# Kernel optimization log

Hardware: AMD Instinct MI355X
Metric: run time of the kernel (lower is better)

## Reference

```python
import jax, jax.numpy as jnp
import numpy as np

NUM_HEADS = 12
ROPE_THETA = 10000.0


def rope_angles(hd, end_x, end_y):
    # axial 2D rope angles, shape (L, hd//2); first hd//4 from x-coord, next hd//4 from y-coord
    f = 1.0 / (ROPE_THETA ** (np.arange(0, hd, 4)[: hd // 4].astype(np.float32) / hd))
    t = np.arange(end_x * end_y)
    tx = (t % end_x).astype(np.float32)
    ty = (t // end_x).astype(np.float32)
    ang = np.concatenate([np.outer(tx, f), np.outer(ty, f)], axis=-1)
    return jnp.asarray(ang, dtype=jnp.float32)


def apply_rope(q, ang):
    # q: (B, nH, L, hd); complex multiply on adjacent pairs
    cos, sin = jnp.cos(ang), jnp.sin(ang)  # (L, hd//2)
    qr = q.reshape(*q.shape[:-1], -1, 2)
    a, b = qr[..., 0], qr[..., 1]
    return jnp.stack([a * cos - b * sin, a * sin + b * cos], axis=-1).reshape(q.shape)


def setup_inputs() -> dict:
    key = jax.random.key(0)
    ks = jax.random.split(key, 7)
    dim, H, W, B = 768, 32, 32, 8
    hd = dim // NUM_HEADS
    return {
        "x": jax.random.normal(ks[0], (B, H, W, dim), jnp.float32),
        "qkv_w": jax.random.normal(ks[1], (3 * dim, dim), jnp.float32) * 0.02,
        "qkv_b": jax.random.normal(ks[2], (3 * dim,), jnp.float32) * 0.02,
        "proj_w": jax.random.normal(ks[3], (dim, dim), jnp.float32) * 0.02,
        "proj_b": jax.random.normal(ks[4], (dim,), jnp.float32) * 0.02,
        "rel_pos_h": jax.random.normal(ks[5], (2 * H - 1, hd), jnp.float32) * 0.02,
        "rel_pos_w": jax.random.normal(ks[6], (2 * W - 1, hd), jnp.float32) * 0.02,
    }


def reference(x, qkv_w, qkv_b, proj_w, proj_b, rel_pos_h, rel_pos_w):
    B, H, W, dim = x.shape
    nH = NUM_HEADS
    hd = dim // nH
    L = H * W
    qkv = jnp.einsum("blc,dc->bld", x.reshape(B, L, dim), qkv_w) + qkv_b
    qkv = qkv.reshape(B, L, 3, nH, hd)
    q = qkv[:, :, 0].transpose(0, 2, 1, 3)  # (B, nH, L, hd)
    k = qkv[:, :, 1].transpose(0, 2, 1, 3)
    v = qkv[:, :, 2].transpose(0, 2, 1, 3)
    # 2D rope (applied to both q and k)
    ang = rope_angles(hd, H, W)
    q = apply_rope(q, ang)
    k = apply_rope(k, ang)
    # relative position bias: equivalent math of concat_rel_pos(rescale=True) + SDPA
    # effective scores = (q.k)/sqrt(hd) + rel_h + rel_w
    rc = jnp.arange(H)[:, None] - jnp.arange(W)[None, :] + (H - 1)  # (H, W)
    Rh = rel_pos_h[rc]  # (H, K_h, hd)
    Rw = rel_pos_w[rc]  # (W, K_w, hd)
    rq = q.reshape(B, nH, H, W, hd)
    rel_h = jnp.einsum("bnhwc,hkc->bnhwk", rq, Rh)  # (B, nH, H, W, K_h)
    rel_w = jnp.einsum("bnhwc,wkc->bnhwk", rq, Rw)  # (B, nH, H, W, K_w)
    scores = jnp.einsum("bnqc,bnkc->bnqk", q, k) / jnp.sqrt(jnp.float32(hd))
    scores = scores.reshape(B, nH, H, W, H, W) + rel_h[..., :, None] + rel_w[..., None, :]
    attn = jax.nn.softmax(scores.reshape(B, nH, L, L), axis=-1)
    out = jnp.einsum("bnqk,bnkc->bnqc", attn, v)  # (B, nH, L, hd)
    out = out.transpose(0, 2, 1, 3).reshape(B, H, W, dim)
    return jnp.einsum("bhwc,dc->bhwd", out, proj_w) + proj_b
```

## Files before the change

kernel.cpp:

```cpp
#include <hip/hip_runtime.h>


typedef unsigned short u16;
typedef __attribute__((ext_vector_type(8))) __bf16 bf16x8;
typedef __attribute__((ext_vector_type(4))) float f32x4;
typedef __attribute__((address_space(1))) const unsigned int gu32;
typedef __attribute__((address_space(3))) unsigned int lu32;

#define LOG2E 1.4426950408889634f

__device__ __forceinline__ float b2f(u16 u) {
    unsigned int i = ((unsigned int)u) << 16;
    float f; __builtin_memcpy(&f, &i, 4); return f;
}
__device__ __forceinline__ u16 f2b(float f) {
    unsigned int x; __builtin_memcpy(&x, &f, 4);
    x += 0x7fffu + ((x >> 16) & 1u);
    return (u16)(x >> 16);
}

#define LDT 72

__global__ void detect_dtype(const u16* __restrict__ x, int* __restrict__ flag)
{
    if (threadIdx.x == 0 && blockIdx.x == 0) {
        float mx = 0.f;
        for (int i = 0; i < 128; i++) {
            float v = fabsf(b2f(x[i]));
            if (!(v <= 1e30f)) v = 1e30f;
            mx = fmaxf(mx, v);
        }
        *flag = (mx > 1e4f) ? 1 : 0;
    }
}

struct CvtArgs {
    const void* src[7];
    u16*        dst[7];
    int         n[7];
    float       sc[7];
};

__global__ __launch_bounds__(256) void convert_all(CvtArgs a, const int* __restrict__ flag)
{
    const int fl = *flag;
    const int g = blockIdx.x * 256 + threadIdx.x;
    const int stride = gridDim.x * 256;
    #pragma unroll 1
    for (int s = 0; s < 7; s++) {
        const int n = a.n[s];
        const float sc = a.sc[s];
        const float* fs = (const float*)a.src[s];
        const u16*  hs = (const u16*)a.src[s];
        u16* d = a.dst[s];
        for (int i = g; i < n; i += stride) {
            float v = fl ? fs[i] : b2f(hs[i]);
            d[i] = f2b(v * sc);
        }
    }
}

template <int EPI>
__global__ __launch_bounds__(256) void gemm128(
    const u16* __restrict__ A, const u16* __restrict__ Bw,
    const u16* __restrict__ bias, void* __restrict__ Cout,
    const int* __restrict__ flag, u16* __restrict__ qkvT, int N, int K)
{
    __shared__ __align__(16) u16 smem[16384];
    u16* lA = smem;
    u16* lB = smem + 8192;
    u16* ct = smem;
    const int tid = threadIdx.x;
    const int m0 = blockIdx.x * 128, n0 = blockIdx.y * 128;
    const int wave = tid >> 6, lane = tid & 63;
    const int wm = (wave & 1) * 64, wn = (wave >> 1) * 64;
    const int lm = lane & 15, lq = lane >> 4;
    const int srow = lane >> 3;
    const int sgcol = ((lane & 7) ^ (srow & 7)) * 8;
    const int sw0 = (lq ^ (lm & 7)) * 8;
    const int sw1 = ((lq + 4) ^ (lm & 7)) * 8;
    f32x4 acc[4][4] = {};
    for (int k0 = 0; k0 < K; k0 += 64) {
        if (k0) __syncthreads();
        #pragma unroll
        for (int c4 = 0; c4 < 4; c4++) {
            const int c = wave * 4 + c4;
            const int row = c * 8 + srow;
            __builtin_amdgcn_global_load_lds(
                (gu32*)(A + (size_t)(m0 + row) * K + k0 + sgcol),
                (lu32*)&lA[c * 512], 16, 0, 0);
            __builtin_amdgcn_global_load_lds(
                (gu32*)(Bw + (size_t)(n0 + row) * K + k0 + sgcol),
                (lu32*)&lB[c * 512], 16, 0, 0);
        }
        __syncthreads();
        #pragma unroll
        for (int ks = 0; ks < 64; ks += 32) {
            const int sw = ks ? sw1 : sw0;
            bf16x8 af[4], bfr[4];
            #pragma unroll
            for (int i = 0; i < 4; i++) af[i]  = *(const bf16x8*)&lA[(wm + i * 16 + lm) * 64 + sw];
            #pragma unroll
            for (int j = 0; j < 4; j++) bfr[j] = *(const bf16x8*)&lB[(wn + j * 16 + lm) * 64 + sw];
            #pragma unroll
            for (int i = 0; i < 4; i++)
                #pragma unroll
                for (int j = 0; j < 4; j++)
                    acc[i][j] = __builtin_amdgcn_mfma_f32_16x16x32_bf16(af[i], bfr[j], acc[i][j], 0, 0, 0);
        }
    }
    if (EPI == 0) {
        const int fl = *flag;
        #pragma unroll
        for (int j = 0; j < 4; j++) {
            const int n = n0 + wn + j * 16 + lm;
            const float bj = b2f(bias[n]);
            #pragma unroll
            for (int i = 0; i < 4; i++)
                #pragma unroll
                for (int r = 0; r < 4; r++) {
                    const int m = m0 + wm + i * 16 + lq * 4 + r;
                    const float v = acc[i][j][r] + bj;
                    if (fl) ((float*)Cout)[(size_t)m * 768 + n] = v;
                    else    ((u16*)Cout)[(size_t)m * 768 + n] = f2b(v);
                }
        }
    } else {
        const int which = n0 / 768;
        const bool vt = (which == 2);
        __syncthreads();
        #pragma unroll
        for (int j = 0; j < 4; j++) {
            const int nl = wn + j * 16 + lm;
            const int n = n0 + nl;
            const float bj = b2f(bias[n]);
            #pragma unroll
            for (int i = 0; i < 4; i++)
                #pragma unroll
                for (int r = 0; r < 4; r++) {
                    const int ml = wm + i * 16 + lq * 4 + r;
                    const int m = m0 + ml;
                    float v = acc[i][j][r] + bj;
                    const float p = __shfl_xor(v, 1);
                    const int l = m & 1023, d = n & 63;
                    float o = v;
                    if (which < 2) {
                        const int pi = d >> 1, jj = pi & 15;
                        const float coord = (pi < 16) ? (float)(l & 31) : (float)(l >> 5);
                        const float ang = coord * __expf(-(float)jj * 0.5756462732485115f);
                        float sn, cs; __sincosf(ang, &sn, &cs);
                        o = v * cs + ((d & 1) ? p * sn : -(p * sn));
                        if (which == 1) o *= 0.125f * LOG2E;
                    }
                    ct[vt ? nl * 128 + ml : ml * 128 + nl] = f2b(o);
                }
        }
        __syncthreads();
        const size_t HL = (size_t)96 * 1024 * 64;
        const int nh0 = (n0 >> 6) % 12, bb = m0 >> 10, l0 = m0 & 1023;
        if (!vt) {
            #pragma unroll
            for (int pass = 0; pass < 8; pass++) {
                const int chunk = pass * 256 + tid;
                const int run = chunk >> 3, lc = chunk & 7;
                const int ml = run >> 1, h = run & 1;
                u16* gp = qkvT + (size_t)which * HL
                        + ((size_t)(bb * 12 + nh0 + h) * 1024 + l0 + ml) * 64 + lc * 8;
                *(uint4*)gp = *(const uint4*)&ct[ml * 128 + h * 64 + lc * 8];
            }
        } else {
            const int kt0 = l0 >> 6;
            #pragma unroll
            for (int pass = 0; pass < 8; pass++) {
                const int run = pass * 16 + (tid >> 4);
                const int ln = tid & 15;
                const int half = ln >> 3, l8 = ln & 7;
                u16* gp = qkvT + 2 * HL
                        + (size_t)(bb * 12 + nh0 + (run >> 6)) * 65536
                        + (size_t)(kt0 + half) * 4096 + (run & 63) * 64 + l8 * 8;
                *(uint4*)gp = *(const uint4*)&ct[run * 128 + ln * 8];
            }
        }
    }
}

__global__ __launch_bounds__(256) void flash_attn_mfma(
    const u16* __restrict__ qkvT, const u16* __restrict__ relH,
    const u16* __restrict__ relW, u16* __restrict__ outb)
{
    __shared__ __align__(16) u16 ks2[2 * 4096];
    __shared__ __align__(16) u16 vsT[2 * 4096];
    __shared__ __align__(16) u16 pq[4096];
    __shared__ __align__(16) u16 ThL[64 * 66];
    u16* rel = vsT;

    const int tid = threadIdx.x;
    const int w = tid >> 6, lane = tid & 63;
    const int lm = lane & 15, lq = lane >> 4;
    const int srow = lane >> 3;
    const int sgcol = ((lane & 7) ^ (srow & 7)) * 8;
    const int sw0 = (lq ^ (lm & 7)) * 8;
    const int sw1 = ((lq + 4) ^ (lm & 7)) * 8;

    const int bn = blockIdx.x, q0 = blockIdx.y * 64;
    const size_t HL = (size_t)96 * 1024 * 64;
    const u16* qg  = qkvT + (size_t)bn * 65536 + (size_t)q0 * 64;
    const u16* kgb = qkvT + HL + (size_t)bn * 65536;
    const u16* vgb = qkvT + 2 * HL + (size_t)bn * 65536;

    #pragma unroll
    for (int c4 = 0; c4 < 2; c4++) {
        const int c = w * 2 + c4;
        const int row = c * 8 + srow;
        __builtin_amdgcn_global_load_lds(
            (gu32*)(qg + row * 64 + sgcol), (lu32*)&pq[c * 512], 16, 0, 0);
    }
    for (int g = tid; g < 1008; g += 256) {
        int r = g >> 4, c = (g & 15) * 4;
        *(ushort4*)&rel[r * 64 + c] = *(const ushort4*)(relH + g * 4);
    }
    if (tid < 16) { ushort4 z = {0, 0, 0, 0}; *(ushort4*)&rel[63 * 64 + tid * 4] = z; }
    __syncthreads();

    const bf16x8 bq0 = *(const bf16x8*)&pq[(w * 16 + lm) * 64 + sw0];
    const bf16x8 bq1 = *(const bf16x8*)&pq[(w * 16 + lm) * 64 + sw1];

    {
        f32x4 tacc[4] = {};
        #pragma unroll
        for (int nb = 0; nb < 4; nb++) {
            bf16x8 r0 = *(const bf16x8*)&rel[(nb * 16 + lm) * 64 + lq * 8];
            bf16x8 r1 = *(const bf16x8*)&rel[(nb * 16 + lm) * 64 + 32 + lq * 8];
            tacc[nb] = __builtin_amdgcn_mfma_f32_16x16x32_bf16(bq0, r0, tacc[nb], 0, 0, 0);
            tacc[nb] = __builtin_amdgcn_mfma_f32_16x16x32_bf16(bq1, r1, tacc[nb], 0, 0, 0);
        }
        #pragma unroll
        for (int nb = 0; nb < 4; nb++)
            #pragma unroll
            for (int rr = 0; rr < 4; rr++)
                ThL[(w * 16 + lq * 4 + rr) * 66 + nb * 16 + lm] = f2b(tacc[nb][rr]);
    }
    __syncthreads();
    for (int g = tid; g < 1008; g += 256) {
        int r = g >> 4, c = (g & 15) * 4;
        *(ushort4*)&rel[r * 64 + c] = *(const ushort4*)(relW + g * 4);
    }
    if (tid < 16) { ushort4 z = {0, 0, 0, 0}; *(ushort4*)&rel[63 * 64 + tid * 4] = z; }
    __syncthreads();
    {
        f32x4 tacc[4] = {};
        #pragma unroll
        for (int nb = 0; nb < 4; nb++) {
            bf16x8 r0 = *(const bf16x8*)&rel[(nb * 16 + lm) * 64 + lq * 8];
            bf16x8 r1 = *(const bf16x8*)&rel[(nb * 16 + lm) * 64 + 32 + lq * 8];
            tacc[nb] = __builtin_amdgcn_mfma_f32_16x16x32_bf16(bq0, r0, tacc[nb], 0, 0, 0);
            tacc[nb] = __builtin_amdgcn_mfma_f32_16x16x32_bf16(bq1, r1, tacc[nb], 0, 0, 0);
        }
        #pragma unroll
        for (int nb = 0; nb < 4; nb++)
            #pragma unroll
            for (int rr = 0; rr < 4; rr++)
                ks2[(w * 16 + lq * 4 + rr) * 66 + nb * 16 + lm] = f2b(tacc[nb][rr]);
    }
    __syncthreads();
    const int qw = (w & 1) * 16 + lm;
    float rwc[8];
    #pragma unroll
    for (int mb2 = 0; mb2 < 2; mb2++)
        #pragma unroll
        for (int rr = 0; rr < 4; rr++) {
            const int kw = mb2 * 16 + lq * 4 + rr;
            rwc[mb2 * 4 + rr] = b2f(ks2[(w * 16 + lm) * 66 + qw - kw + 31]) - 16.0f;
        }
    const int qh = (q0 >> 5) + (w >= 2 ? 1 : 0);

    union { unsigned u[4]; bf16x8 v; } uo;
    uo.u[0] = uo.u[1] = uo.u[2] = uo.u[3] = 0x3F803F80u;
    const bf16x8 vone = uo.v;

    f32x4 lacc = {};
    f32x4 oacc[4] = {};

    __syncthreads();
    #pragma unroll
    for (int c4 = 0; c4 < 2; c4++) {
        const int c = w * 2 + c4;
        const int row = c * 8 + srow;
        __builtin_amdgcn_global_load_lds(
            (gu32*)(kgb + row * 64 + sgcol), (lu32*)&ks2[c * 512], 16, 0, 0);
        __builtin_amdgcn_global_load_lds(
            (gu32*)(vgb + row * 64 + sgcol), (lu32*)&vsT[c * 512], 16, 0, 0);
    }

    #pragma unroll 1
    for (int kt = 0; kt < 16; kt++) {
        __syncthreads();
        const int bo = (kt & 1) * 4096;
        if (kt < 15) {
            const int bn1 = ((kt + 1) & 1) * 4096;
            const u16* kp = kgb + (size_t)(kt + 1) * 4096;
            const u16* vp = vgb + (size_t)(kt + 1) * 4096;
            #pragma unroll
            for (int c4 = 0; c4 < 2; c4++) {
                const int c = w * 2 + c4;
                const int row = c * 8 + srow;
                __builtin_amdgcn_global_load_lds(
                    (gu32*)(kp + row * 64 + sgcol), (lu32*)&ks2[bn1 + c * 512], 16, 0, 0);
                __builtin_amdgcn_global_load_lds(
                    (gu32*)(vp + row * 64 + sgcol), (lu32*)&vsT[bn1 + c * 512], 16, 0, 0);
            }
        }
        f32x4 sacc[4];
        #pragma unroll
        for (int mb = 0; mb < 4; mb++) {
            bf16x8 ka0 = *(const bf16x8*)&ks2[bo + (mb * 16 + lm) * 64 + sw0];
            bf16x8 ka1 = *(const bf16x8*)&ks2[bo + (mb * 16 + lm) * 64 + sw1];
            f32x4 s = {};
            s = __builtin_amdgcn_mfma_f32_16x16x32_bf16(ka0, bq0, s, 0, 0, 0);
            s = __builtin_amdgcn_mfma_f32_16x16x32_bf16(ka1, bq1, s, 0, 0, 0);
            sacc[mb] = s;
        }
        const float rh0 = b2f(ThL[(w * 16 + lm) * 66 + qh - 2 * kt + 31]);
        const float rh1 = b2f(ThL[(w * 16 + lm) * 66 + qh - 2 * kt + 30]);
        #pragma unroll
        for (int mb = 0; mb < 4; mb++) {
            const float rhv = (mb >= 2) ? rh1 : rh0;
            float p0 = exp2f(sacc[mb][0] + rhv + rwc[(mb & 1) * 4 + 0]);
            float p1 = exp2f(sacc[mb][1] + rhv + rwc[(mb & 1) * 4 + 1]);
            float p2 = exp2f(sacc[mb][2] + rhv + rwc[(mb & 1) * 4 + 2]);
            float p3 = exp2f(sacc[mb][3] + rhv + rwc[(mb & 1) * 4 + 3]);
            unsigned w0, w1;
            asm("v_cvt_pk_bf16_f32 %0, %1, %2" : "=v"(w0) : "v"(p0), "v"(p1));
            asm("v_cvt_pk_bf16_f32 %0, %1, %2" : "=v"(w1) : "v"(p2), "v"(p3));
            uint2 u; u.x = w0; u.y = w1;
            const int gg = 2 * mb + (lq >> 1);
            *(uint2*)&pq[(w * 16 + lm) * 64 + ((gg ^ (lm & 7)) * 8) + (lq & 1) * 4] = u;
        }
        const bf16x8 pa0 = *(const bf16x8*)&pq[(w * 16 + lm) * 64 + sw0];
        const bf16x8 pa1 = *(const bf16x8*)&pq[(w * 16 + lm) * 64 + sw1];
        lacc = __builtin_amdgcn_mfma_f32_16x16x32_bf16(pa0, vone, lacc, 0, 0, 0);
        lacc = __builtin_amdgcn_mfma_f32_16x16x32_bf16(pa1, vone, lacc, 0, 0, 0);
        #pragma unroll
        for (int nb = 0; nb < 4; nb++) {
            bf16x8 vb0 = *(const bf16x8*)&vsT[bo + (nb * 16 + lm) * 64 + sw0];
            bf16x8 vb1 = *(const bf16x8*)&vsT[bo + (nb * 16 + lm) * 64 + sw1];
            oacc[nb] = __builtin_amdgcn_mfma_f32_16x16x32_bf16(pa0, vb0, oacc[nb], 0, 0, 0);
            oacc[nb] = __builtin_amdgcn_mfma_f32_16x16x32_bf16(pa1, vb1, oacc[nb], 0, 0, 0);
        }
    }
    float rv[4];
    #pragma unroll
    for (int rr = 0; rr < 4; rr++) rv[rr] = 1.f / lacc[rr];
    const int bb = bn / 12, nh = bn % 12;
    #pragma unroll
    for (int nb = 0; nb < 4; nb++)
        #pragma unroll
        for (int rr = 0; rr < 4; rr++) {
            const int qrow = q0 + w * 16 + lq * 4 + rr;
            const int d = nb * 16 + lm;
            outb[((size_t)(bb * 1024 + qrow)) * 768 + nh * 64 + d] = f2b(oacc[nb][rr] * rv[rr]);
        }
}

extern "C" void kernel_launch(void* const* d_in, const int* in_sizes, int n_in,
                              void* d_out, int out_size, void* d_ws, size_t ws_size,
                              hipStream_t stream)
{
    u16* ws16  = (u16*)d_ws;
    u16* qkvT  = ws16;
    u16* xb    = ws16 + (size_t)18874368;
    u16* attn  = xb;
    const size_t S = 25165824;
    u16* qkvw_b = ws16 + S;
    u16* projw_b = qkvw_b + 1769472;
    u16* qkvb_b = projw_b + 589824;
    u16* projb_b = qkvb_b + 2304;
    u16* relh_b = projb_b + 768;
    u16* relw_b = relh_b + 4032;
    int* flag = (int*)(ws16 + S + 2370432);

    detect_dtype<<<1, 64, 0, stream>>>((const u16*)d_in[0], flag);

    CvtArgs ca;
    ca.src[0] = d_in[0]; ca.dst[0] = xb;      ca.n[0] = 6291456; ca.sc[0] = 1.0f;
    ca.src[1] = d_in[1]; ca.dst[1] = qkvw_b;  ca.n[1] = 1769472; ca.sc[1] = 1.0f;
    ca.src[2] = d_in[3]; ca.dst[2] = projw_b; ca.n[2] = 589824;  ca.sc[2] = 1.0f;
    ca.src[3] = d_in[2]; ca.dst[3] = qkvb_b;  ca.n[3] = 2304;    ca.sc[3] = 1.0f;
    ca.src[4] = d_in[4]; ca.dst[4] = projb_b; ca.n[4] = 768;     ca.sc[4] = 1.0f;
    ca.src[5] = d_in[5]; ca.dst[5] = relh_b;  ca.n[5] = 4032;    ca.sc[5] = LOG2E;
    ca.src[6] = d_in[6]; ca.dst[6] = relw_b;  ca.n[6] = 4032;    ca.sc[6] = LOG2E;
    convert_all<<<2048, 256, 0, stream>>>(ca, flag);

    gemm128<1><<<dim3(64, 18), 256, 0, stream>>>(xb, qkvw_b, qkvb_b, nullptr, flag, qkvT, 2304, 768);
    flash_attn_mfma<<<dim3(96, 16), 256, 0, stream>>>(qkvT, relh_b, relw_b, attn);
    gemm128<0><<<dim3(64, 6), 256, 0, stream>>>(attn, projw_b, projb_b, d_out, flag, nullptr, 768, 768);
}
```

Baseline: 233.7 us.

## Process two query halves per attention block and tabulate rope sin/cos

Measured after the change: 225.1 us. 1.04x faster.

```diff
diff --git a/kernel.cpp b/kernel.cpp
--- a/kernel.cpp
+++ b/kernel.cpp
@@ -18,8 +18,6 @@
     x += 0x7fffu + ((x >> 16) & 1u);
     return (u16)(x >> 16);
 }
-
-#define LDT 72
 
 __global__ void detect_dtype(const u16* __restrict__ x, int* __restrict__ flag)
 {
@@ -67,6 +65,8 @@
     const int* __restrict__ flag, u16* __restrict__ qkvT, int N, int K)
 {
     __shared__ __align__(16) u16 smem[16384];
+    __shared__ float tabc[512];
+    __shared__ float tabs[512];
     u16* lA = smem;
     u16* lB = smem + 8192;
     u16* ct = smem;
@@ -79,6 +79,17 @@
     const int sgcol = ((lane & 7) ^ (srow & 7)) * 8;
     const int sw0 = (lq ^ (lm & 7)) * 8;
     const int sw1 = ((lq + 4) ^ (lm & 7)) * 8;
+
+    if (EPI == 1) {
+        #pragma unroll
+        for (int e = tid; e < 512; e += 256) {
+            const int coord = e >> 4, jj = e & 15;
+            const float ang = (float)coord * __expf(-(float)jj * 0.5756462732485115f);
+            float sn, cs; __sincosf(ang, &sn, &cs);
+            tabc[e] = cs; tabs[e] = sn;
+        }
+    }
+
     f32x4 acc[4][4] = {};
     for (int k0 = 0; k0 < K; k0 += 64) {
         if (k0) __syncthreads();
@@ -134,6 +145,9 @@
             const int nl = wn + j * 16 + lm;
             const int n = n0 + nl;
             const float bj = b2f(bias[n]);
+            const int d = n & 63;
+            const int pi = d >> 1;
+            const int jj = pi & 15;
             #pragma unroll
             for (int i = 0; i < 4; i++)
                 #pragma unroll
@@ -142,13 +156,12 @@
                     const int m = m0 + ml;
                     float v = acc[i][j][r] + bj;
                     const float p = __shfl_xor(v, 1);
-                    const int l = m & 1023, d = n & 63;
+                    const int l = m & 1023;
                     float o = v;
                     if (which < 2) {
-                        const int pi = d >> 1, jj = pi & 15;
-                        const float coord = (pi < 16) ? (float)(l & 31) : (float)(l >> 5);
-                        const float ang = coord * __expf(-(float)jj * 0.5756462732485115f);
-                        float sn, cs; __sincosf(ang, &sn, &cs);
+                        const int coord = (pi < 16) ? (l & 31) : (l >> 5);
+                        const float cs = tabc[coord * 16 + jj];
+                        const float sn = tabs[coord * 16 + jj];
                         o = v * cs + ((d & 1) ? p * sn : -(p * sn));
                         if (which == 1) o *= 0.125f * LOG2E;
                     }
@@ -184,37 +197,41 @@
     }
 }
 
-__global__ __launch_bounds__(256) void flash_attn_mfma(
+__global__ __launch_bounds__(256, 3) void flash_attn_mfma(
     const u16* __restrict__ qkvT, const u16* __restrict__ relH,
     const u16* __restrict__ relW, u16* __restrict__ outb)
 {
     __shared__ __align__(16) u16 ks2[2 * 4096];
     __shared__ __align__(16) u16 vsT[2 * 4096];
-    __shared__ __align__(16) u16 pq[4096];
-    __shared__ __align__(16) u16 ThL[64 * 66];
+    __shared__ __align__(16) u16 ps[4096];
+    __shared__ __align__(16) u16 ThL[128 * 36];
     u16* rel = vsT;
+    u16* TwS = ks2;
 
     const int tid = threadIdx.x;
     const int w = tid >> 6, lane = tid & 63;
     const int lm = lane & 15, lq = lane >> 4;
+    const int whi = (w >= 2) ? 1 : 0;
     const int srow = lane >> 3;
     const int sgcol = ((lane & 7) ^ (srow & 7)) * 8;
     const int sw0 = (lq ^ (lm & 7)) * 8;
     const int sw1 = ((lq + 4) ^ (lm & 7)) * 8;
 
-    const int bn = blockIdx.x, q0 = blockIdx.y * 64;
+    const int bn = blockIdx.x, q0 = blockIdx.y * 128;
+    const int qh0 = blockIdx.y * 4;
     const size_t HL = (size_t)96 * 1024 * 64;
     const u16* qg  = qkvT + (size_t)bn * 65536 + (size_t)q0 * 64;
     const u16* kgb = qkvT + HL + (size_t)bn * 65536;
     const u16* vgb = qkvT + 2 * HL + (size_t)bn * 65536;
 
+    bf16x8 bq0[2], bq1[2];
     #pragma unroll
-    for (int c4 = 0; c4 < 2; c4++) {
-        const int c = w * 2 + c4;
-        const int row = c * 8 + srow;
-        __builtin_amdgcn_global_load_lds(
-            (gu32*)(qg + row * 64 + sgcol), (lu32*)&pq[c * 512], 16, 0, 0);
-    }
+    for (int h = 0; h < 2; h++) {
+        const u16* qr = qg + (h * 64 + w * 16 + lm) * 64;
+        bq0[h] = *(const bf16x8*)(qr + lq * 8);
+        bq1[h] = *(const bf16x8*)(qr + 32 + lq * 8);
+    }
+
     for (int g = tid; g < 1008; g += 256) {
         int r = g >> 4, c = (g & 15) * 4;
         *(ushort4*)&rel[r * 64 + c] = *(const ushort4*)(relH + g * 4);
@@ -222,23 +239,26 @@
     if (tid < 16) { ushort4 z = {0, 0, 0, 0}; *(ushort4*)&rel[63 * 64 + tid * 4] = z; }
     __syncthreads();
 
-    const bf16x8 bq0 = *(const bf16x8*)&pq[(w * 16 + lm) * 64 + sw0];
-    const bf16x8 bq1 = *(const bf16x8*)&pq[(w * 16 + lm) * 64 + sw1];
-
     {
-        f32x4 tacc[4] = {};
-        #pragma unroll
-        for (int nb = 0; nb < 4; nb++) {
-            bf16x8 r0 = *(const bf16x8*)&rel[(nb * 16 + lm) * 64 + lq * 8];
-            bf16x8 r1 = *(const bf16x8*)&rel[(nb * 16 + lm) * 64 + 32 + lq * 8];
-            tacc[nb] = __builtin_amdgcn_mfma_f32_16x16x32_bf16(bq0, r0, tacc[nb], 0, 0, 0);
-            tacc[nb] = __builtin_amdgcn_mfma_f32_16x16x32_bf16(bq1, r1, tacc[nb], 0, 0, 0);
-        }
-        #pragma unroll
-        for (int nb = 0; nb < 4; nb++)
-            #pragma unroll
-            for (int rr = 0; rr < 4; rr++)
-                ThL[(w * 16 + lq * 4 + rr) * 66 + nb * 16 + lm] = f2b(tacc[nb][rr]);
+        #pragma unroll
+        for (int h = 0; h < 2; h++) {
+            f32x4 tacc[4] = {};
+            #pragma unroll
+            for (int nb = 0; nb < 4; nb++) {
+                bf16x8 r0 = *(const bf16x8*)&rel[(nb * 16 + lm) * 64 + lq * 8];
+                bf16x8 r1 = *(const bf16x8*)&rel[(nb * 16 + lm) * 64 + 32 + lq * 8];
+                tacc[nb] = __builtin_amdgcn_mfma_f32_16x16x32_bf16(bq0[h], r0, tacc[nb], 0, 0, 0);
+                tacc[nb] = __builtin_amdgcn_mfma_f32_16x16x32_bf16(bq1[h], r1, tacc[nb], 0, 0, 0);
+            }
+            #pragma unroll
+            for (int nb = 0; nb < 4; nb++)
+                #pragma unroll
+                for (int rr = 0; rr < 4; rr++) {
+                    const unsigned cw = (unsigned)(nb * 16 + lm - qh0);
+                    if (cw < 36u)
+                        ThL[(h * 64 + w * 16 + lq * 4 + rr) * 36 + cw] = f2b(tacc[nb][rr]);
+                }
+        }
     }
     __syncthreads();
     for (int g = tid; g < 1008; g += 256) {
@@ -248,38 +268,43 @@
     if (tid < 16) { ushort4 z = {0, 0, 0, 0}; *(ushort4*)&rel[63 * 64 + tid * 4] = z; }
     __syncthreads();
     {
-        f32x4 tacc[4] = {};
-        #pragma unroll
-        for (int nb = 0; nb < 4; nb++) {
-            bf16x8 r0 = *(const bf16x8*)&rel[(nb * 16 + lm) * 64 + lq * 8];
-            bf16x8 r1 = *(const bf16x8*)&rel[(nb * 16 + lm) * 64 + 32 + lq * 8];
-            tacc[nb] = __builtin_amdgcn_mfma_f32_16x16x32_bf16(bq0, r0, tacc[nb], 0, 0, 0);
-            tacc[nb] = __builtin_amdgcn_mfma_f32_16x16x32_bf16(bq1, r1, tacc[nb], 0, 0, 0);
-        }
-        #pragma unroll
-        for (int nb = 0; nb < 4; nb++)
-            #pragma unroll
-            for (int rr = 0; rr < 4; rr++)
-                ks2[(w * 16 + lq * 4 + rr) * 66 + nb * 16 + lm] = f2b(tacc[nb][rr]);
+        #pragma unroll
+        for (int h = 0; h < 2; h++) {
+            f32x4 tacc[4] = {};
+            #pragma unroll
+            for (int nb = 0; nb < 4; nb++) {
+                bf16x8 r0 = *(const bf16x8*)&rel[(nb * 16 + lm) * 64 + lq * 8];
+                bf16x8 r1 = *(const bf16x8*)&rel[(nb * 16 + lm) * 64 + 32 + lq * 8];
+                tacc[nb] = __builtin_amdgcn_mfma_f32_16x16x32_bf16(bq0[h], r0, tacc[nb], 0, 0, 0);
+                tacc[nb] = __builtin_amdgcn_mfma_f32_16x16x32_bf16(bq1[h], r1, tacc[nb], 0, 0, 0);
+            }
+            #pragma unroll
+            for (int nb = 0; nb < 4; nb++)
+                #pragma unroll
+                for (int rr = 0; rr < 4; rr++)
+                    TwS[(h * 64 + w * 16 + lq * 4 + rr) * 64 + nb * 16 + lm] = f2b(tacc[nb][rr]);
+        }
     }
     __syncthreads();
     const int qw = (w & 1) * 16 + lm;
-    float rwc[8];
+    float rwc[2][8];
     #pragma unroll
-    for (int mb2 = 0; mb2 < 2; mb2++)
-        #pragma unroll
-        for (int rr = 0; rr < 4; rr++) {
-            const int kw = mb2 * 16 + lq * 4 + rr;
-            rwc[mb2 * 4 + rr] = b2f(ks2[(w * 16 + lm) * 66 + qw - kw + 31]) - 16.0f;
-        }
-    const int qh = (q0 >> 5) + (w >= 2 ? 1 : 0);
+    for (int h = 0; h < 2; h++)
+        #pragma unroll
+        for (int mb2 = 0; mb2 < 2; mb2++)
+            #pragma unroll
+            for (int rr = 0; rr < 4; rr++) {
+                const int kw = mb2 * 16 + lq * 4 + rr;
+                rwc[h][mb2 * 4 + rr] =
+                    b2f(TwS[(h * 64 + w * 16 + lm) * 64 + qw - kw + 31]) - 16.0f;
+            }
 
     union { unsigned u[4]; bf16x8 v; } uo;
     uo.u[0] = uo.u[1] = uo.u[2] = uo.u[3] = 0x3F803F80u;
     const bf16x8 vone = uo.v;
 
-    f32x4 lacc = {};
-    f32x4 oacc[4] = {};
+    f32x4 lacc[2] = {};
+    f32x4 oacc[2][4] = {};
 
     __syncthreads();
     #pragma unroll
@@ -310,56 +335,72 @@
                     (gu32*)(vp + row * 64 + sgcol), (lu32*)&vsT[bn1 + c * 512], 16, 0, 0);
             }
         }
-        f32x4 sacc[4];
+        float rh[2][2];
+        #pragma unroll
+        for (int h = 0; h < 2; h++) {
+            const int colp = h * 2 + whi - 2 * kt + 31;
+            rh[h][0] = b2f(ThL[(h * 64 + w * 16 + lm) * 36 + colp]);
+            rh[h][1] = b2f(ThL[(h * 64 + w * 16 + lm) * 36 + colp - 1]);
+        }
+        bf16x8 ka0[4], ka1[4];
         #pragma unroll
         for (int mb = 0; mb < 4; mb++) {
-            bf16x8 ka0 = *(const bf16x8*)&ks2[bo + (mb * 16 + lm) * 64 + sw0];
-            bf16x8 ka1 = *(const bf16x8*)&ks2[bo + (mb * 16 + lm) * 64 + sw1];
-            f32x4 s = {};
-            s = __builtin_amdgcn_mfma_f32_16x16x32_bf16(ka0, bq0, s, 0, 0, 0);
-            s = __builtin_amdgcn_mfma_f32_16x16x32_bf16(ka1, bq1, s, 0, 0, 0);
-            sacc[mb] = s;
-        }
-        const float rh0 = b2f(ThL[(w * 16 + lm) * 66 + qh - 2 * kt + 31]);
-        const float rh1 = b2f(ThL[(w * 16 + lm) * 66 + qh - 2 * kt + 30]);
-        #pragma unroll
-        for (int mb = 0; mb < 4; mb++) {
-            const float rhv = (mb >= 2) ? rh1 : rh0;
-            float p0 = exp2f(sacc[mb][0] + rhv + rwc[(mb & 1) * 4 + 0]);
-            float p1 = exp2f(sacc[mb][1] + rhv + rwc[(mb & 1) * 4 + 1]);
-            float p2 = exp2f(sacc[mb][2] + rhv + rwc[(mb & 1) * 4 + 2]);
-            float p3 = exp2f(sacc[mb][3] + rhv + rwc[(mb & 1) * 4 + 3]);
-            unsigned w0, w1;
-            asm("v_cvt_pk_bf16_f32 %0, %1, %2" : "=v"(w0) : "v"(p0), "v"(p1));
-            asm("v_cvt_pk_bf16_f32 %0, %1, %2" : "=v"(w1) : "v"(p2), "v"(p3));
-            uint2 u; u.x = w0; u.y = w1;
-            const int gg = 2 * mb + (lq >> 1);
-            *(uint2*)&pq[(w * 16 + lm) * 64 + ((gg ^ (lm & 7)) * 8) + (lq & 1) * 4] = u;
-        }
-        const bf16x8 pa0 = *(const bf16x8*)&pq[(w * 16 + lm) * 64 + sw0];
-        const bf16x8 pa1 = *(const bf16x8*)&pq[(w * 16 + lm) * 64 + sw1];
-        lacc = __builtin_amdgcn_mfma_f32_16x16x32_bf16(pa0, vone, lacc, 0, 0, 0);
-        lacc = __builtin_amdgcn_mfma_f32_16x16x32_bf16(pa1, vone, lacc, 0, 0, 0);
-        #pragma unroll
-        for (int nb = 0; nb < 4; nb++) {
-            bf16x8 vb0 = *(const bf16x8*)&vsT[bo + (nb * 16 + lm) * 64 + sw0];
-            bf16x8 vb1 = *(const bf16x8*)&vsT[bo + (nb * 16 + lm) * 64 + sw1];
-            oacc[nb] = __builtin_amdgcn_mfma_f32_16x16x32_bf16(pa0, vb0, oacc[nb], 0, 0, 0);
-            oacc[nb] = __builtin_amdgcn_mfma_f32_16x16x32_bf16(pa1, vb1, oacc[nb], 0, 0, 0);
-        }
-    }
-    float rv[4];
-    #pragma unroll
-    for (int rr = 0; rr < 4; rr++) rv[rr] = 1.f / lacc[rr];
+            ka0[mb] = *(const bf16x8*)&ks2[bo + (mb * 16 + lm) * 64 + sw0];
+            ka1[mb] = *(const bf16x8*)&ks2[bo + (mb * 16 + lm) * 64 + sw1];
+        }
+        #pragma unroll
+        for (int h = 0; h < 2; h++) {
+            f32x4 sacc[4];
+            #pragma unroll
+            for (int mb = 0; mb < 4; mb++) {
+                #pragma unroll
+                for (int j = 0; j < 4; j++)
+                    sacc[mb][j] = rh[h][mb >> 1] + rwc[h][(mb & 1) * 4 + j];
+                sacc[mb] = __builtin_amdgcn_mfma_f32_16x16x32_bf16(ka0[mb], bq0[h], sacc[mb], 0, 0, 0);
+                sacc[mb] = __builtin_amdgcn_mfma_f32_16x16x32_bf16(ka1[mb], bq1[h], sacc[mb], 0, 0, 0);
+            }
+            #pragma unroll
+            for (int mb = 0; mb < 4; mb++) {
+                float p0 = exp2f(sacc[mb][0]);
+                float p1 = exp2f(sacc[mb][1]);
+                float p2 = exp2f(sacc[mb][2]);
+                float p3 = exp2f(sacc[mb][3]);
+                unsigned w0, w1;
+                asm("v_cvt_pk_bf16_f32 %0, %1, %2" : "=v"(w0) : "v"(p0), "v"(p1));
+                asm("v_cvt_pk_bf16_f32 %0, %1, %2" : "=v"(w1) : "v"(p2), "v"(p3));
+                uint2 u; u.x = w0; u.y = w1;
+                const int gg = 2 * mb + (lq >> 1);
+                *(uint2*)&ps[(w * 16 + lm) * 64 + ((gg ^ (lm & 7)) * 8) + (lq & 1) * 4] = u;
+            }
+            const bf16x8 pa0 = *(const bf16x8*)&ps[(w * 16 + lm) * 64 + sw0];
+            const bf16x8 pa1 = *(const bf16x8*)&ps[(w * 16 + lm) * 64 + sw1];
+            lacc[h] = __builtin_amdgcn_mfma_f32_16x16x32_bf16(pa0, vone, lacc[h], 0, 0, 0);
+            lacc[h] = __builtin_amdgcn_mfma_f32_16x16x32_bf16(pa1, vone, lacc[h], 0, 0, 0);
+            #pragma unroll
+            for (int nb = 0; nb < 4; nb++) {
+                bf16x8 vb0 = *(const bf16x8*)&vsT[bo + (nb * 16 + lm) * 64 + sw0];
+                bf16x8 vb1 = *(const bf16x8*)&vsT[bo + (nb * 16 + lm) * 64 + sw1];
+                oacc[h][nb] = __builtin_amdgcn_mfma_f32_16x16x32_bf16(pa0, vb0, oacc[h][nb], 0, 0, 0);
+                oacc[h][nb] = __builtin_amdgcn_mfma_f32_16x16x32_bf16(pa1, vb1, oacc[h][nb], 0, 0, 0);
+            }
+        }
+    }
     const int bb = bn / 12, nh = bn % 12;
     #pragma unroll
-    for (int nb = 0; nb < 4; nb++)
-        #pragma unroll
-        for (int rr = 0; rr < 4; rr++) {
-            const int qrow = q0 + w * 16 + lq * 4 + rr;
-            const int d = nb * 16 + lm;
-            outb[((size_t)(bb * 1024 + qrow)) * 768 + nh * 64 + d] = f2b(oacc[nb][rr] * rv[rr]);
-        }
+    for (int h = 0; h < 2; h++) {
+        float rv[4];
+        #pragma unroll
+        for (int rr = 0; rr < 4; rr++) rv[rr] = 1.f / lacc[h][rr];
+        #pragma unroll
+        for (int nb = 0; nb < 4; nb++)
+            #pragma unroll
+            for (int rr = 0; rr < 4; rr++) {
+                const int qrow = q0 + h * 64 + w * 16 + lq * 4 + rr;
+                const int d = nb * 16 + lm;
+                outb[((size_t)(bb * 1024 + qrow)) * 768 + nh * 64 + d] =
+                    f2b(oacc[h][nb][rr] * rv[rr]);
+            }
+    }
 }
 
 extern "C" void kernel_launch(void* const* d_in, const int* in_sizes, int n_in,
@@ -392,6 +433,6 @@
     convert_all<<<2048, 256, 0, stream>>>(ca, flag);
 
     gemm128<1><<<dim3(64, 18), 256, 0, stream>>>(xb, qkvw_b, qkvb_b, nullptr, flag, qkvT, 2304, 768);
-    flash_attn_mfma<<<dim3(96, 16), 256, 0, stream>>>(qkvT, relh_b, relw_b, attn);
+    flash_attn_mfma<<<dim3(96, 8), 256, 0, stream>>>(qkvT, relh_b, relw_b, attn);
     gemm128<0><<<dim3(64, 6), 256, 0, stream>>>(attn, projw_b, projb_b, d_out, flag, nullptr, 768, 768);
 }
```
